# Kernel tuning notes

Hardware: AMD Instinct MI355X
Metric: run time of the kernel (lower is better)

The kernel has to match this reference:

```python
import jax, jax.numpy as jnp
import numpy as np

N, IN, OUT = 262144, 256, 256


def setup_inputs() -> dict:
    key = jax.random.key(0)
    k1, k2, k3 = jax.random.split(key, 3)
    x = jax.random.normal(k1, (N, IN), dtype=jnp.float32)
    weight = jax.random.normal(k2, (OUT, IN), dtype=jnp.float32) * 0.01
    scale = jax.random.uniform(k3, (1, OUT), dtype=jnp.float32) * 0.1
    return {"x": x, "weight": weight, "scale": scale}


def reference(x, weight, scale):
    # XNOR-Net style: binarize activations and weights via sign(),
    # float matmul, then per-output-channel scale.
    xb = jnp.sign(x)            # [N, IN]
    wb = jnp.sign(weight)       # [OUT, IN]
    y = jnp.einsum('ni,oi->no', xb, wb)  # F.linear
    return y * scale            # broadcast [1, OUT] over rows
```

## Files before the change

kernel.cpp:

```cpp
#include <hip/hip_runtime.h>


#define N_ROWS 262144
#define IN_DIM 256
#define OUT_DIM 256
#define ROWS_PER_WAVE 64

typedef unsigned long long u64;

__global__ void pack_weights(const float* __restrict__ w, u64* __restrict__ wb) {
    const int o = blockIdx.x;
    const int l = threadIdx.x;
    const float4 f = ((const float4*)(w + (size_t)o * IN_DIM))[l];
    u64 b0 = __ballot(f.x < 0.0f);
    u64 b1 = __ballot(f.y < 0.0f);
    u64 b2 = __ballot(f.z < 0.0f);
    u64 b3 = __ballot(f.w < 0.0f);
    if (l == 0) {
        wb[o * 4 + 0] = b0;
        wb[o * 4 + 1] = b1;
        wb[o * 4 + 2] = b2;
        wb[o * 4 + 3] = b3;
    }
}

__global__ void __launch_bounds__(256, 4) bin_linear(
    const float* __restrict__ x, const u64* __restrict__ wb,
    const float* __restrict__ scale, float* __restrict__ out)
{
    const int l  = threadIdx.x & 63;
    const int wv = threadIdx.x >> 6;
    const int gw = blockIdx.x * 4 + wv;

    u64 W[4][4];
#pragma unroll
    for (int j = 0; j < 4; ++j) {
#pragma unroll
        for (int s = 0; s < 4; ++s) {
            W[j][s] = wb[(size_t)(4 * l + j) * 4 + s];
        }
    }
    const float4 sc = ((const float4*)scale)[l];

    const int row0 = gw * ROWS_PER_WAVE;
    const float4* xp = (const float4*)(x + (size_t)row0 * IN_DIM) + l;
    float4*       op = (float4*)(out + (size_t)row0 * IN_DIM) + l;

    float4 cur = *xp;
#pragma unroll 4
    for (int i = 0; i < ROWS_PER_WAVE; ++i) {
        float4 nxt = cur;
        if (i + 1 < ROWS_PER_WAVE) nxt = xp[(i + 1) * (IN_DIM / 4)];

        const u64 b0 = __ballot(cur.x < 0.0f);
        const u64 b1 = __ballot(cur.y < 0.0f);
        const u64 b2 = __ballot(cur.z < 0.0f);
        const u64 b3 = __ballot(cur.w < 0.0f);

        float4 o4;
        {
            int h = __builtin_popcountll(b0 ^ W[0][0]) + __builtin_popcountll(b1 ^ W[0][1])
                  + __builtin_popcountll(b2 ^ W[0][2]) + __builtin_popcountll(b3 ^ W[0][3]);
            o4.x = (float)(IN_DIM - 2 * h) * sc.x;
        }
        {
            int h = __builtin_popcountll(b0 ^ W[1][0]) + __builtin_popcountll(b1 ^ W[1][1])
                  + __builtin_popcountll(b2 ^ W[1][2]) + __builtin_popcountll(b3 ^ W[1][3]);
            o4.y = (float)(IN_DIM - 2 * h) * sc.y;
        }
        {
            int h = __builtin_popcountll(b0 ^ W[2][0]) + __builtin_popcountll(b1 ^ W[2][1])
                  + __builtin_popcountll(b2 ^ W[2][2]) + __builtin_popcountll(b3 ^ W[2][3]);
            o4.z = (float)(IN_DIM - 2 * h) * sc.z;
        }
        {
            int h = __builtin_popcountll(b0 ^ W[3][0]) + __builtin_popcountll(b1 ^ W[3][1])
                  + __builtin_popcountll(b2 ^ W[3][2]) + __builtin_popcountll(b3 ^ W[3][3]);
            o4.w = (float)(IN_DIM - 2 * h) * sc.w;
        }

        op[i * (IN_DIM / 4)] = o4;
        cur = nxt;
    }
}

extern "C" void kernel_launch(void* const* d_in, const int* in_sizes, int n_in,
                              void* d_out, int out_size, void* d_ws, size_t ws_size,
                              hipStream_t stream) {
    const float* x     = (const float*)d_in[0];
    const float* wgt   = (const float*)d_in[1];
    const float* scale = (const float*)d_in[2];
    float* out = (float*)d_out;
    u64* wb = (u64*)d_ws;

    pack_weights<<<OUT_DIM, 64, 0, stream>>>(wgt, wb);
    bin_linear<<<N_ROWS / 256, 256, 0, stream>>>(x, wb, scale, out);
}
```

Measured before the change: 453.5 us.

## Deepen load pipeline to four rows with nontemporal loads and stores, halve rows per wave

Each wave now keeps four rows of x in flight through a rotating register buffer instead of prefetching one row ahead. Loads and stores use nontemporal builtins to avoid polluting cache on streaming data. Rows per wave are halved, doubling the grid. This targets the memory latency that bounds a 256MB streaming read and 256MB write, at the cost of more registers and more repeated weight-mask loads.

```diff
diff --git a/kernel.cpp b/kernel.cpp
--- a/kernel.cpp
+++ b/kernel.cpp
@@ -4,9 +4,11 @@
 #define N_ROWS 262144
 #define IN_DIM 256
 #define OUT_DIM 256
-#define ROWS_PER_WAVE 64
+#define ROWS_PER_WAVE 32
+#define PIPE 4
 
 typedef unsigned long long u64;
+typedef float f32x4 __attribute__((ext_vector_type(4)));
 
 __global__ void pack_weights(const float* __restrict__ w, u64* __restrict__ wb) {
     const int o = blockIdx.x;
@@ -24,6 +26,35 @@
     }
 }
 
+__device__ __forceinline__ f32x4 row_dot(f32x4 cur, const u64 W[4][4], f32x4 sc) {
+    const u64 b0 = __ballot(cur.x < 0.0f);
+    const u64 b1 = __ballot(cur.y < 0.0f);
+    const u64 b2 = __ballot(cur.z < 0.0f);
+    const u64 b3 = __ballot(cur.w < 0.0f);
+    f32x4 o4;
+    {
+        int h = __builtin_popcountll(b0 ^ W[0][0]) + __builtin_popcountll(b1 ^ W[0][1])
+              + __builtin_popcountll(b2 ^ W[0][2]) + __builtin_popcountll(b3 ^ W[0][3]);
+        o4.x = (float)(IN_DIM - 2 * h) * sc.x;
+    }
+    {
+        int h = __builtin_popcountll(b0 ^ W[1][0]) + __builtin_popcountll(b1 ^ W[1][1])
+              + __builtin_popcountll(b2 ^ W[1][2]) + __builtin_popcountll(b3 ^ W[1][3]);
+        o4.y = (float)(IN_DIM - 2 * h) * sc.y;
+    }
+    {
+        int h = __builtin_popcountll(b0 ^ W[2][0]) + __builtin_popcountll(b1 ^ W[2][1])
+              + __builtin_popcountll(b2 ^ W[2][2]) + __builtin_popcountll(b3 ^ W[2][3]);
+        o4.z = (float)(IN_DIM - 2 * h) * sc.z;
+    }
+    {
+        int h = __builtin_popcountll(b0 ^ W[3][0]) + __builtin_popcountll(b1 ^ W[3][1])
+              + __builtin_popcountll(b2 ^ W[3][2]) + __builtin_popcountll(b3 ^ W[3][3]);
+        o4.w = (float)(IN_DIM - 2 * h) * sc.w;
+    }
+    return o4;
+}
+
 __global__ void __launch_bounds__(256, 4) bin_linear(
     const float* __restrict__ x, const u64* __restrict__ wb,
     const float* __restrict__ scale, float* __restrict__ out)
@@ -34,53 +65,32 @@
 
     u64 W[4][4];
 #pragma unroll
-    for (int j = 0; j < 4; ++j) {
+    for (int j = 0; j < 4; ++j)
 #pragma unroll
-        for (int s = 0; s < 4; ++s) {
+        for (int s = 0; s < 4; ++s)
             W[j][s] = wb[(size_t)(4 * l + j) * 4 + s];
-        }
-    }
-    const float4 sc = ((const float4*)scale)[l];
+
+    const f32x4 sc = ((const f32x4*)scale)[l];
 
     const int row0 = gw * ROWS_PER_WAVE;
-    const float4* xp = (const float4*)(x + (size_t)row0 * IN_DIM) + l;
-    float4*       op = (float4*)(out + (size_t)row0 * IN_DIM) + l;
+    const f32x4* xp = (const f32x4*)(x + (size_t)row0 * IN_DIM) + l;
+    f32x4*       op = (f32x4*)(out + (size_t)row0 * IN_DIM) + l;
+    const int rstride = IN_DIM / 4;
 
-    float4 cur = *xp;
+    f32x4 buf[PIPE];
+#pragma unroll
+    for (int p = 0; p < PIPE; ++p)
+        buf[p] = __builtin_nontemporal_load(&xp[p * rstride]);
+
 #pragma unroll 4
-    for (int i = 0; i < ROWS_PER_WAVE; ++i) {
-        float4 nxt = cur;
-        if (i + 1 < ROWS_PER_WAVE) nxt = xp[(i + 1) * (IN_DIM / 4)];
-
-        const u64 b0 = __ballot(cur.x < 0.0f);
-        const u64 b1 = __ballot(cur.y < 0.0f);
-        const u64 b2 = __ballot(cur.z < 0.0f);
-        const u64 b3 = __ballot(cur.w < 0.0f);
-
-        float4 o4;
-        {
-            int h = __builtin_popcountll(b0 ^ W[0][0]) + __builtin_popcountll(b1 ^ W[0][1])
-                  + __builtin_popcountll(b2 ^ W[0][2]) + __builtin_popcountll(b3 ^ W[0][3]);
-            o4.x = (float)(IN_DIM - 2 * h) * sc.x;
-        }
-        {
-            int h = __builtin_popcountll(b0 ^ W[1][0]) + __builtin_popcountll(b1 ^ W[1][1])
-                  + __builtin_popcountll(b2 ^ W[1][2]) + __builtin_popcountll(b3 ^ W[1][3]);
-            o4.y = (float)(IN_DIM - 2 * h) * sc.y;
-        }
-        {
-            int h = __builtin_popcountll(b0 ^ W[2][0]) + __builtin_popcountll(b1 ^ W[2][1])
-                  + __builtin_popcountll(b2 ^ W[2][2]) + __builtin_popcountll(b3 ^ W[2][3]);
-            o4.z = (float)(IN_DIM - 2 * h) * sc.z;
-        }
-        {
-            int h = __builtin_popcountll(b0 ^ W[3][0]) + __builtin_popcountll(b1 ^ W[3][1])
-                  + __builtin_popcountll(b2 ^ W[3][2]) + __builtin_popcountll(b3 ^ W[3][3]);
-            o4.w = (float)(IN_DIM - 2 * h) * sc.w;
-        }
-
-        op[i * (IN_DIM / 4)] = o4;
-        cur = nxt;
+    for (int i = 0; i < ROWS_PER_WAVE - PIPE; ++i) {
+        f32x4 cur = buf[i & (PIPE - 1)];
+        buf[i & (PIPE - 1)] = __builtin_nontemporal_load(&xp[(i + PIPE) * rstride]);
+        __builtin_nontemporal_store(row_dot(cur, W, sc), &op[i * rstride]);
+    }
+#pragma unroll
+    for (int i = ROWS_PER_WAVE - PIPE; i < ROWS_PER_WAVE; ++i) {
+        __builtin_nontemporal_store(row_dot(buf[i & (PIPE - 1)], W, sc), &op[i * rstride]);
     }
 }
 
@@ -94,5 +104,5 @@
     u64* wb = (u64*)d_ws;
 
     pack_weights<<<OUT_DIM, 64, 0, stream>>>(wgt, wb);
-    bin_linear<<<N_ROWS / 256, 256, 0, stream>>>(x, wb, scale, out);
+    bin_linear<<<N_ROWS / (4 * ROWS_PER_WAVE), 256, 0, stream>>>(x, wb, scale, out);
 }
```

Result: faster. 432.6 us (-4.6%).
